# Kernel tuning notes

Measured on AMD Instinct MI355X. Metric: run time of the kernel, lower is better.

The kernel has to match this reference:

```python
import jax, jax.numpy as jnp
import numpy as np

SIMS = 16
AMP = 1.0  # cfg['attention_amplifier']


def setup_inputs() -> dict:
    key = jax.random.key(0)
    k1, k2, k3 = jax.random.split(key, 3)
    B, F = 32, 2048
    data = jax.random.normal(k1, (B * SIMS, F), dtype=jnp.float32)
    attention = jax.random.normal(k2, (B * SIMS, F), dtype=jnp.float32)
    W = jax.random.normal(k3, (SIMS, 2 * SIMS), dtype=jnp.float32) * (1.0 / np.sqrt(2 * SIMS))
    b = jnp.zeros((SIMS,), dtype=jnp.float32)
    return {"data": data, "attention": attention, "W": W, "b": b}


def reference(data, attention, W, b):
    s = SIMS
    B = data.shape[0] // s
    inputs = data.reshape(B, s, -1)            # [B, s, F]
    attn_in = attention.reshape(B, s, -1)      # [B, s, G]
    # bmm(inputs^T, attention) -> [B, F, G]
    a = jnp.einsum('bsf,bsg->bfg', inputs, attn_in)
    a = jax.nn.log_softmax(a, axis=1)          # log_softmax over F dim (dim=1)
    # bmm(a, attention^T) -> [B, F, s]
    a = jnp.einsum('bfg,bsg->bfs', a, attn_in)
    concat = jnp.concatenate([jnp.swapaxes(a, 1, 2), inputs], axis=1)  # [B, 2s, F]
    concat = jnp.swapaxes(concat, 1, 2).reshape(-1, 2 * s)             # [B*F, 2s]
    gate = jax.nn.sigmoid(concat @ W.T + b)    # [B*F, s]
    # output.t().contiguous().view(data.shape): [s, B*F] row-major -> [B*s, F]
    gate = gate.T.reshape(data.shape)
    return gate * data * AMP
```

## Files before the change

### kernel.cpp

```cpp
#include <hip/hip_runtime.h>
#include <math.h>

#define LOG2E 1.44269504088896340736f
#define LN2   0.69314718055994530942f

typedef _Float16 half8 __attribute__((ext_vector_type(8)));
typedef float f32x4v __attribute__((ext_vector_type(4)));

#define AROW 24

template <bool ATOMIC>
__global__ __launch_bounds__(256, 4) void kA(const float* __restrict__ data,
                                             const float* __restrict__ attn,
                                             float* __restrict__ Lout) {
    __shared__ _Float16 AhB[128 * AROW];
    __shared__ _Float16 AlB[128 * AROW];
    const int tid = threadIdx.x;
    const int b = blockIdx.z, fb = blockIdx.y, gb = blockIdx.x;
    const int wave = tid >> 6, lane = tid & 63;
    const int n = lane & 15, q = lane >> 4;
    const int s0 = (q & 1) * 8;

    const float* Tb = attn + (size_t)b * 16 * 2048;
    half8 B1[2], B2[2];
#pragma unroll
    for (int ct = 0; ct < 2; ++ct) {
        const int g = gb * 128 + wave * 32 + ct * 16 + n;
        half8 bh, bl;
#pragma unroll
        for (int j = 0; j < 8; ++j) {
            float x = Tb[(size_t)(s0 + j) * 2048 + g] * LOG2E;
            _Float16 h = (_Float16)x;
            _Float16 l = (_Float16)(x - (float)h);
            bh[j] = h;
            bl[j] = (q < 2) ? l : (_Float16)0.0f;
        }
        B1[ct] = bh;
        B2[ct] = bl;
    }

    f32x4v cs0 = {0.f, 0.f, 0.f, 0.f}, cs1 = {0.f, 0.f, 0.f, 0.f};

    const float* Ab = data + (size_t)b * 16 * 2048 + fb * 512;
    const int fst = tid & 127;
    const int sh  = (tid >> 7) * 8;
    const _Float16* aptr = ((q < 2) ? AhB : AlB) + n * AROW + s0;

    for (int chunk = 0; chunk < 4; ++chunk) {
        const float* Ac = Ab + chunk * 128;
        _Float16 hb[8], lb[8];
#pragma unroll
        for (int j = 0; j < 8; ++j) {
            float x = Ac[(size_t)(sh + j) * 2048 + fst];
            _Float16 h = (_Float16)x;
            hb[j] = h;
            lb[j] = (_Float16)(x - (float)h);
        }
        __syncthreads();
        half8 hv, lv;
#pragma unroll
        for (int j = 0; j < 8; ++j) { hv[j] = hb[j]; lv[j] = lb[j]; }
        *(half8*)(AhB + fst * AROW + sh) = hv;
        *(half8*)(AlB + fst * AROW + sh) = lv;
        __syncthreads();

#pragma unroll
        for (int rt = 0; rt < 8; ++rt) {
            half8 af = *(const half8*)(aptr + rt * 16 * AROW);
            f32x4v C = {0.f, 0.f, 0.f, 0.f};
            C = __builtin_amdgcn_mfma_f32_16x16x32_f16(af, B1[0], C, 0, 0, 0);
            C = __builtin_amdgcn_mfma_f32_16x16x32_f16(af, B2[0], C, 0, 0, 0);
            cs0[0] += __builtin_amdgcn_exp2f(C[0]);
            cs0[1] += __builtin_amdgcn_exp2f(C[1]);
            cs0[2] += __builtin_amdgcn_exp2f(C[2]);
            cs0[3] += __builtin_amdgcn_exp2f(C[3]);
            f32x4v D = {0.f, 0.f, 0.f, 0.f};
            D = __builtin_amdgcn_mfma_f32_16x16x32_f16(af, B1[1], D, 0, 0, 0);
            D = __builtin_amdgcn_mfma_f32_16x16x32_f16(af, B2[1], D, 0, 0, 0);
            cs1[0] += __builtin_amdgcn_exp2f(D[0]);
            cs1[1] += __builtin_amdgcn_exp2f(D[1]);
            cs1[2] += __builtin_amdgcn_exp2f(D[2]);
            cs1[3] += __builtin_amdgcn_exp2f(D[3]);
        }
    }

    float v0 = cs0[0] + cs0[1] + cs0[2] + cs0[3];
    float v1 = cs1[0] + cs1[1] + cs1[2] + cs1[3];
    v0 += __shfl_xor(v0, 16);
    v0 += __shfl_xor(v0, 32);
    v1 += __shfl_xor(v1, 16);
    v1 += __shfl_xor(v1, 32);
    if (q == 0) {
        const int g = gb * 128 + wave * 32 + n;
        if (ATOMIC) {
            atomicAdd(&Lout[(size_t)b * 2048 + g], v0);
            atomicAdd(&Lout[(size_t)b * 2048 + g + 16], v1);
        } else {
            Lout[((size_t)fb * 32 + b) * 2048 + g] = v0;
            Lout[((size_t)fb * 32 + b) * 2048 + g + 16] = v1;
        }
    }
}

#define TP 260
__global__ __launch_bounds__(256) void kTail(const float* __restrict__ attn,
                                             const float* __restrict__ Lpart, int nparts,
                                             float* __restrict__ Mpart,
                                             float* __restrict__ cpart) {
    __shared__ float Tsh[16 * TP];
    __shared__ float Lsh[256];
    __shared__ float red[16][17];
    const int tid = threadIdx.x;
    const int seg = blockIdx.x, b = blockIdx.y;
    const int g0 = seg * 256;

#pragma unroll
    for (int s = 0; s < 16; ++s)
        Tsh[s * TP + tid] = attn[(size_t)(b * 16 + s) * 2048 + g0 + tid];
    {
        float sum = 0.f;
        for (int p = 0; p < nparts; ++p)
            sum += Lpart[((size_t)p * 32 + b) * 2048 + g0 + tid];
        Lsh[tid] = LN2 * __builtin_amdgcn_logf(sum);
    }
    __syncthreads();

    {
        const int t = tid & 15, i = tid >> 4;
        float acc = 0.f;
#pragma unroll
        for (int k = 0; k < 4; ++k) {
            float4 l  = *(const float4*)(Lsh + i * 16 + k * 4);
            float4 tv = *(const float4*)(Tsh + t * TP + i * 16 + k * 4);
            acc += l.x * tv.x + l.y * tv.y + l.z * tv.z + l.w * tv.w;
        }
        red[t][i] = acc;
    }
    __syncthreads();
    if (tid < 16) {
        float s = 0.f;
#pragma unroll
        for (int k = 0; k < 16; ++k) s += red[tid][k];
        cpart[((size_t)seg * 32 + b) * 16 + tid] = s;
    }

    {
        const int s = tid >> 4, t = tid & 15;
        float a0 = 0.f, a1 = 0.f;
#pragma unroll 4
        for (int qk = 0; qk < 32; ++qk) {
            float4 x = *(const float4*)(Tsh + s * TP + qk * 8);
            float4 y = *(const float4*)(Tsh + t * TP + qk * 8);
            a0 += x.x * y.x + x.y * y.y + x.z * y.z + x.w * y.w;
            float4 x2 = *(const float4*)(Tsh + s * TP + qk * 8 + 4);
            float4 y2 = *(const float4*)(Tsh + t * TP + qk * 8 + 4);
            a1 += x2.x * y2.x + x2.y * y2.y + x2.z * y2.z + x2.w * y2.w;
        }
        Mpart[((size_t)seg * 32 + b) * 256 + tid] = a0 + a1;
    }
}

__global__ __launch_bounds__(256) void kC2(const float* __restrict__ data,
                                           const float* __restrict__ Mpart,
                                           const float* __restrict__ cpart,
                                           const float* __restrict__ W,
                                           const float* __restrict__ bias,
                                           float* __restrict__ out) {
    __shared__ float Msh[256];
    __shared__ float csh[16];
    __shared__ float Vsh[256];
    __shared__ float w0sh[16];
    const int tid = threadIdx.x;
    const int b = blockIdx.y;
    const int f = blockIdx.x * 256 + tid;

    {
        float m = 0.f;
#pragma unroll
        for (int p = 0; p < 8; ++p) m += Mpart[((size_t)p * 32 + b) * 256 + tid];
        Msh[tid] = m;
        if (tid < 16) {
            float c = 0.f;
#pragma unroll
            for (int p = 0; p < 8; ++p) c += cpart[((size_t)p * 32 + b) * 16 + tid];
            csh[tid] = c;
        }
    }
    __syncthreads();
    {
        const int s = tid >> 4, j = tid & 15;
        float acc = 0.f;
#pragma unroll
        for (int t = 0; t < 16; ++t) acc += Msh[s * 16 + t] * W[j * 32 + t];
        Vsh[s * 16 + j] = acc + W[j * 32 + 16 + s];
        if (s == 0) {
            float w0 = 0.f;
#pragma unroll
            for (int t = 0; t < 16; ++t) w0 += csh[t] * W[j * 32 + t];
            w0sh[j] = bias[j] - w0;
        }
    }
    __syncthreads();

    float As[16];
#pragma unroll
    for (int s = 0; s < 16; ++s)
        As[s] = data[(size_t)(b * 16 + s) * 2048 + f];
#pragma unroll
    for (int j = 0; j < 16; ++j) {
        float p = w0sh[j];
#pragma unroll
        for (int s = 0; s < 16; ++s) p += As[s] * Vsh[s * 16 + j];
        float e = __builtin_amdgcn_exp2f(-LOG2E * p);
        float gate = __builtin_amdgcn_rcpf(1.0f + e);
        size_t r = (size_t)(j * 32 + b) * 2048 + f;
        out[r] = gate * data[r];
    }
}

extern "C" void kernel_launch(void* const* d_in, const int* in_sizes, int n_in,
                              void* d_out, int out_size, void* d_ws, size_t ws_size,
                              hipStream_t stream) {
    const float* data = (const float*)d_in[0];
    const float* attn = (const float*)d_in[1];
    const float* W    = (const float*)d_in[2];
    const float* bias = (const float*)d_in[3];
    float* out = (float*)d_out;
    float* ws  = (float*)d_ws;

    const size_t LP = 4 * 32 * 2048;
    const size_t need_big = LP + 65536 + 4096;

    if (ws_size >= need_big * sizeof(float)) {
        float* Lpart = ws;
        float* Mpart = ws + LP;
        float* cpart = Mpart + 65536;
        kA<false><<<dim3(16, 4, 32), 256, 0, stream>>>(data, attn, Lpart);
        kTail<<<dim3(8, 32), 256, 0, stream>>>(attn, Lpart, 4, Mpart, cpart);
        kC2<<<dim3(8, 32), 256, 0, stream>>>(data, Mpart, cpart, W, bias, out);
    } else {
        float* Lsum  = ws;
        float* Mpart = ws + 65536;
        float* cpart = Mpart + 65536;
        hipMemsetAsync(Lsum, 0, 65536 * sizeof(float), stream);
        kA<true><<<dim3(16, 4, 32), 256, 0, stream>>>(data, attn, Lsum);
        kTail<<<dim3(8, 32), 256, 0, stream>>>(attn, Lsum, 1, Mpart, cpart);
        kC2<<<dim3(8, 32), 256, 0, stream>>>(data, Mpart, cpart, W, bias, out);
    }
}
```

Measured before the change: 94.99 us.

## Double-buffer LDS A tiles and widen kA to 256 columns per block

kA now covers 256 g-columns per block (4 column tiles per wave) instead of 128, which halves the grid and halves redundant loads and fp16 split conversion of the data tile. The shared A buffers become double-buffered so the next chunk's global load overlaps the MFMA and exp2 work on the current chunk, leaving one barrier per chunk. In exchange each thread holds more registers (B fragments, accumulators, prefetch), which may lower occupancy, and the smaller grid gives less parallelism.

After: 219.5 us. +131.0%, slower.

```diff
diff --git a/kernel.cpp b/kernel.cpp
--- a/kernel.cpp
+++ b/kernel.cpp
@@ -13,8 +13,8 @@
 __global__ __launch_bounds__(256, 4) void kA(const float* __restrict__ data,
                                              const float* __restrict__ attn,
                                              float* __restrict__ Lout) {
-    __shared__ _Float16 AhB[128 * AROW];
-    __shared__ _Float16 AlB[128 * AROW];
+    __shared__ _Float16 AhB[2][128 * AROW];
+    __shared__ _Float16 AlB[2][128 * AROW];
     const int tid = threadIdx.x;
     const int b = blockIdx.z, fb = blockIdx.y, gb = blockIdx.x;
     const int wave = tid >> 6, lane = tid & 63;
@@ -22,10 +22,10 @@
     const int s0 = (q & 1) * 8;
 
     const float* Tb = attn + (size_t)b * 16 * 2048;
-    half8 B1[2], B2[2];
-#pragma unroll
-    for (int ct = 0; ct < 2; ++ct) {
-        const int g = gb * 128 + wave * 32 + ct * 16 + n;
+    half8 B1[4], B2[4];
+#pragma unroll
+    for (int ct = 0; ct < 4; ++ct) {
+        const int g = gb * 256 + wave * 64 + ct * 16 + n;
         half8 bh, bl;
 #pragma unroll
         for (int j = 0; j < 8; ++j) {
@@ -39,65 +39,88 @@
         B2[ct] = bl;
     }
 
-    f32x4v cs0 = {0.f, 0.f, 0.f, 0.f}, cs1 = {0.f, 0.f, 0.f, 0.f};
+    f32x4v cs[4];
+#pragma unroll
+    for (int ct = 0; ct < 4; ++ct) cs[ct] = (f32x4v){0.f, 0.f, 0.f, 0.f};
 
     const float* Ab = data + (size_t)b * 16 * 2048 + fb * 512;
     const int fst = tid & 127;
     const int sh  = (tid >> 7) * 8;
-    const _Float16* aptr = ((q < 2) ? AhB : AlB) + n * AROW + s0;
-
-    for (int chunk = 0; chunk < 4; ++chunk) {
-        const float* Ac = Ab + chunk * 128;
-        _Float16 hb[8], lb[8];
+
+    const _Float16* ap0 = ((q < 2) ? &AhB[0][0] : &AlB[0][0]) + n * AROW + s0;
+    const _Float16* ap1 = ((q < 2) ? &AhB[1][0] : &AlB[1][0]) + n * AROW + s0;
+
+    {
+        const float* Ac = Ab;
+        half8 hv, lv;
 #pragma unroll
         for (int j = 0; j < 8; ++j) {
             float x = Ac[(size_t)(sh + j) * 2048 + fst];
             _Float16 h = (_Float16)x;
-            hb[j] = h;
-            lb[j] = (_Float16)(x - (float)h);
-        }
-        __syncthreads();
-        half8 hv, lv;
-#pragma unroll
-        for (int j = 0; j < 8; ++j) { hv[j] = hb[j]; lv[j] = lb[j]; }
-        *(half8*)(AhB + fst * AROW + sh) = hv;
-        *(half8*)(AlB + fst * AROW + sh) = lv;
-        __syncthreads();
-
+            hv[j] = h;
+            lv[j] = (_Float16)(x - (float)h);
+        }
+        *(half8*)(&AhB[0][fst * AROW + sh]) = hv;
+        *(half8*)(&AlB[0][fst * AROW + sh]) = lv;
+    }
+    __syncthreads();
+
+    for (int c = 0; c < 4; ++c) {
+        float xr[8];
+        if (c < 3) {
+            const float* Ac = Ab + (c + 1) * 128;
+#pragma unroll
+            for (int j = 0; j < 8; ++j)
+                xr[j] = Ac[(size_t)(sh + j) * 2048 + fst];
+        }
+
+        const _Float16* aptr = (c & 1) ? ap1 : ap0;
 #pragma unroll
         for (int rt = 0; rt < 8; ++rt) {
             half8 af = *(const half8*)(aptr + rt * 16 * AROW);
-            f32x4v C = {0.f, 0.f, 0.f, 0.f};
-            C = __builtin_amdgcn_mfma_f32_16x16x32_f16(af, B1[0], C, 0, 0, 0);
-            C = __builtin_amdgcn_mfma_f32_16x16x32_f16(af, B2[0], C, 0, 0, 0);
-            cs0[0] += __builtin_amdgcn_exp2f(C[0]);
-            cs0[1] += __builtin_amdgcn_exp2f(C[1]);
-            cs0[2] += __builtin_amdgcn_exp2f(C[2]);
-            cs0[3] += __builtin_amdgcn_exp2f(C[3]);
-            f32x4v D = {0.f, 0.f, 0.f, 0.f};
-            D = __builtin_amdgcn_mfma_f32_16x16x32_f16(af, B1[1], D, 0, 0, 0);
-            D = __builtin_amdgcn_mfma_f32_16x16x32_f16(af, B2[1], D, 0, 0, 0);
-            cs1[0] += __builtin_amdgcn_exp2f(D[0]);
-            cs1[1] += __builtin_amdgcn_exp2f(D[1]);
-            cs1[2] += __builtin_amdgcn_exp2f(D[2]);
-            cs1[3] += __builtin_amdgcn_exp2f(D[3]);
-        }
-    }
-
-    float v0 = cs0[0] + cs0[1] + cs0[2] + cs0[3];
-    float v1 = cs1[0] + cs1[1] + cs1[2] + cs1[3];
-    v0 += __shfl_xor(v0, 16);
-    v0 += __shfl_xor(v0, 32);
-    v1 += __shfl_xor(v1, 16);
-    v1 += __shfl_xor(v1, 32);
-    if (q == 0) {
-        const int g = gb * 128 + wave * 32 + n;
-        if (ATOMIC) {
-            atomicAdd(&Lout[(size_t)b * 2048 + g], v0);
-            atomicAdd(&Lout[(size_t)b * 2048 + g + 16], v1);
-        } else {
-            Lout[((size_t)fb * 32 + b) * 2048 + g] = v0;
-            Lout[((size_t)fb * 32 + b) * 2048 + g + 16] = v1;
+            f32x4v Cr[4];
+#pragma unroll
+            for (int ct = 0; ct < 4; ++ct) {
+                f32x4v t = {0.f, 0.f, 0.f, 0.f};
+                t = __builtin_amdgcn_mfma_f32_16x16x32_f16(af, B1[ct], t, 0, 0, 0);
+                t = __builtin_amdgcn_mfma_f32_16x16x32_f16(af, B2[ct], t, 0, 0, 0);
+                Cr[ct] = t;
+            }
+#pragma unroll
+            for (int ct = 0; ct < 4; ++ct) {
+                cs[ct][0] += __builtin_amdgcn_exp2f(Cr[ct][0]);
+                cs[ct][1] += __builtin_amdgcn_exp2f(Cr[ct][1]);
+                cs[ct][2] += __builtin_amdgcn_exp2f(Cr[ct][2]);
+                cs[ct][3] += __builtin_amdgcn_exp2f(Cr[ct][3]);
+            }
+        }
+
+        if (c < 3) {
+            half8 hv, lv;
+#pragma unroll
+            for (int j = 0; j < 8; ++j) {
+                _Float16 h = (_Float16)xr[j];
+                hv[j] = h;
+                lv[j] = (_Float16)(xr[j] - (float)h);
+            }
+            const int nb = (c + 1) & 1;
+            *(half8*)(&AhB[nb][fst * AROW + sh]) = hv;
+            *(half8*)(&AlB[nb][fst * AROW + sh]) = lv;
+        }
+        __syncthreads();
+    }
+
+#pragma unroll
+    for (int ct = 0; ct < 4; ++ct) {
+        float v = cs[ct][0] + cs[ct][1] + cs[ct][2] + cs[ct][3];
+        v += __shfl_xor(v, 16);
+        v += __shfl_xor(v, 32);
+        if (q == 0) {
+            const int g = gb * 256 + wave * 64 + ct * 16 + n;
+            if (ATOMIC)
+                atomicAdd(&Lout[(size_t)b * 2048 + g], v);
+            else
+                Lout[((size_t)fb * 32 + b) * 2048 + g] = v;
         }
     }
 }
@@ -235,7 +258,7 @@
         float* Lpart = ws;
         float* Mpart = ws + LP;
         float* cpart = Mpart + 65536;
-        kA<false><<<dim3(16, 4, 32), 256, 0, stream>>>(data, attn, Lpart);
+        kA<false><<<dim3(8, 4, 32), 256, 0, stream>>>(data, attn, Lpart);
         kTail<<<dim3(8, 32), 256, 0, stream>>>(attn, Lpart, 4, Mpart, cpart);
         kC2<<<dim3(8, 32), 256, 0, stream>>>(data, Mpart, cpart, W, bias, out);
     } else {
@@ -243,7 +266,7 @@
         float* Mpart = ws + 65536;
         float* cpart = Mpart + 65536;
         hipMemsetAsync(Lsum, 0, 65536 * sizeof(float), stream);
-        kA<true><<<dim3(16, 4, 32), 256, 0, stream>>>(data, attn, Lsum);
+        kA<true><<<dim3(8, 4, 32), 256, 0, stream>>>(data, attn, Lsum);
         kTail<<<dim3(8, 32), 256, 0, stream>>>(attn, Lsum, 1, Mpart, cpart);
         kC2<<<dim3(8, 32), 256, 0, stream>>>(data, Mpart, cpart, W, bias, out);
     }
```

## Swap operand residency in kA: keep data tile in registers, stage attention in LDS

Applied to the files above, without the earlier changes.

Restructures the log-sum-exp kernel so each wave holds its 64 rows of data (split into high and low fp16 parts) in registers, while a 256-column attention tile is staged once in LDS and streamed through. The grid changes from 16x4 to 8x8 tiles per batch, and the per-wave column sums are reduced through shared memory before one store per column. This removes the per-chunk data staging with its double barrier and spreads the exp work differently. In exchange it uses more LDS per block and produces eight partial buffers instead of four, so the tail kernel has more partials to reduce.

Measured after the change: 98.30 us. 1.03x slower.

```diff
diff --git a/kernel.cpp b/kernel.cpp
--- a/kernel.cpp
+++ b/kernel.cpp
@@ -7,98 +7,91 @@
 typedef _Float16 half8 __attribute__((ext_vector_type(8)));
 typedef float f32x4v __attribute__((ext_vector_type(4)));
 
-#define AROW 24
+#define TROW 24
 
 template <bool ATOMIC>
 __global__ __launch_bounds__(256, 4) void kA(const float* __restrict__ data,
                                              const float* __restrict__ attn,
                                              float* __restrict__ Lout) {
-    __shared__ _Float16 AhB[128 * AROW];
-    __shared__ _Float16 AlB[128 * AROW];
+    __shared__ _Float16 ThL[256 * TROW];
+    __shared__ _Float16 TlL[256 * TROW];
+    __shared__ _Float16 zeroH[8];
+    __shared__ float Lw[4][256];
     const int tid = threadIdx.x;
-    const int b = blockIdx.z, fb = blockIdx.y, gb = blockIdx.x;
+    const int b = blockIdx.z, fb = blockIdx.y, gs = blockIdx.x;
     const int wave = tid >> 6, lane = tid & 63;
     const int n = lane & 15, q = lane >> 4;
-    const int s0 = (q & 1) * 8;
-
-    const float* Tb = attn + (size_t)b * 16 * 2048;
-    half8 B1[2], B2[2];
-#pragma unroll
-    for (int ct = 0; ct < 2; ++ct) {
-        const int g = gb * 128 + wave * 32 + ct * 16 + n;
-        half8 bh, bl;
-#pragma unroll
-        for (int j = 0; j < 8; ++j) {
-            float x = Tb[(size_t)(s0 + j) * 2048 + g] * LOG2E;
-            _Float16 h = (_Float16)x;
-            _Float16 l = (_Float16)(x - (float)h);
-            bh[j] = h;
-            bl[j] = (q < 2) ? l : (_Float16)0.0f;
-        }
-        B1[ct] = bh;
-        B2[ct] = bl;
-    }
-
-    f32x4v cs0 = {0.f, 0.f, 0.f, 0.f}, cs1 = {0.f, 0.f, 0.f, 0.f};
-
-    const float* Ab = data + (size_t)b * 16 * 2048 + fb * 512;
-    const int fst = tid & 127;
-    const int sh  = (tid >> 7) * 8;
-    const _Float16* aptr = ((q < 2) ? AhB : AlB) + n * AROW + s0;
-
-    for (int chunk = 0; chunk < 4; ++chunk) {
-        const float* Ac = Ab + chunk * 128;
-        _Float16 hb[8], lb[8];
-#pragma unroll
-        for (int j = 0; j < 8; ++j) {
-            float x = Ac[(size_t)(sh + j) * 2048 + fst];
-            _Float16 h = (_Float16)x;
-            hb[j] = h;
-            lb[j] = (_Float16)(x - (float)h);
-        }
-        __syncthreads();
-        half8 hv, lv;
-#pragma unroll
-        for (int j = 0; j < 8; ++j) { hv[j] = hb[j]; lv[j] = lb[j]; }
-        *(half8*)(AhB + fst * AROW + sh) = hv;
-        *(half8*)(AlB + fst * AROW + sh) = lv;
-        __syncthreads();
-
-#pragma unroll
-        for (int rt = 0; rt < 8; ++rt) {
-            half8 af = *(const half8*)(aptr + rt * 16 * AROW);
+    const int g0 = gs * 256;
+
+    {
+        const float* Tb = attn + (size_t)b * 16 * 2048 + g0;
+        const int gl = tid >> 1;
+        const int sh = (tid & 1) * 8;
+#pragma unroll
+        for (int p = 0; p < 2; ++p) {
+            const int g = gl + p * 128;
+            half8 hv, lv;
+#pragma unroll
+            for (int j = 0; j < 8; ++j) {
+                float x = Tb[(size_t)(sh + j) * 2048 + g] * LOG2E;
+                _Float16 h = (_Float16)x;
+                hv[j] = h;
+                lv[j] = (_Float16)(x - (float)h);
+            }
+            *(half8*)(ThL + g * TROW + sh) = hv;
+            *(half8*)(TlL + g * TROW + sh) = lv;
+        }
+        if (tid < 8) zeroH[tid] = (_Float16)0.0f;
+    }
+
+    half8 A1[4];
+    {
+        const float* Ab = data + (size_t)b * 16 * 2048;
+        const int frow = fb * 256 + wave * 64;
+#pragma unroll
+        for (int r = 0; r < 4; ++r) {
+            half8 a;
+#pragma unroll
+            for (int j = 0; j < 8; ++j) {
+                const int s = (q & 1) * 8 + j;
+                float x = Ab[(size_t)s * 2048 + frow + r * 16 + n];
+                _Float16 h = (_Float16)x;
+                a[j] = (q < 2) ? h : (_Float16)(x - (float)h);
+            }
+            A1[r] = a;
+        }
+    }
+    __syncthreads();
+
+    const _Float16* b1base = ThL + (q & 1) * 8;
+    const _Float16* b2base = (q < 2) ? (TlL + q * 8) : zeroH;
+    const int b2stride = (q < 2) ? TROW : 0;
+
+    for (int gt = 0; gt < 16; ++gt) {
+        const int gp = gt * 16 + n;
+        half8 B1 = *(const half8*)(b1base + gp * TROW);
+        half8 B2 = *(const half8*)(b2base + gp * b2stride);
+        float sum = 0.f;
+#pragma unroll
+        for (int r = 0; r < 4; ++r) {
             f32x4v C = {0.f, 0.f, 0.f, 0.f};
-            C = __builtin_amdgcn_mfma_f32_16x16x32_f16(af, B1[0], C, 0, 0, 0);
-            C = __builtin_amdgcn_mfma_f32_16x16x32_f16(af, B2[0], C, 0, 0, 0);
-            cs0[0] += __builtin_amdgcn_exp2f(C[0]);
-            cs0[1] += __builtin_amdgcn_exp2f(C[1]);
-            cs0[2] += __builtin_amdgcn_exp2f(C[2]);
-            cs0[3] += __builtin_amdgcn_exp2f(C[3]);
-            f32x4v D = {0.f, 0.f, 0.f, 0.f};
-            D = __builtin_amdgcn_mfma_f32_16x16x32_f16(af, B1[1], D, 0, 0, 0);
-            D = __builtin_amdgcn_mfma_f32_16x16x32_f16(af, B2[1], D, 0, 0, 0);
-            cs1[0] += __builtin_amdgcn_exp2f(D[0]);
-            cs1[1] += __builtin_amdgcn_exp2f(D[1]);
-            cs1[2] += __builtin_amdgcn_exp2f(D[2]);
-            cs1[3] += __builtin_amdgcn_exp2f(D[3]);
-        }
-    }
-
-    float v0 = cs0[0] + cs0[1] + cs0[2] + cs0[3];
-    float v1 = cs1[0] + cs1[1] + cs1[2] + cs1[3];
-    v0 += __shfl_xor(v0, 16);
-    v0 += __shfl_xor(v0, 32);
-    v1 += __shfl_xor(v1, 16);
-    v1 += __shfl_xor(v1, 32);
-    if (q == 0) {
-        const int g = gb * 128 + wave * 32 + n;
-        if (ATOMIC) {
-            atomicAdd(&Lout[(size_t)b * 2048 + g], v0);
-            atomicAdd(&Lout[(size_t)b * 2048 + g + 16], v1);
-        } else {
-            Lout[((size_t)fb * 32 + b) * 2048 + g] = v0;
-            Lout[((size_t)fb * 32 + b) * 2048 + g + 16] = v1;
-        }
+            C = __builtin_amdgcn_mfma_f32_16x16x32_f16(A1[r], B1, C, 0, 0, 0);
+            C = __builtin_amdgcn_mfma_f32_16x16x32_f16(A1[r], B2, C, 0, 0, 0);
+            sum += __builtin_amdgcn_exp2f(C[0]) + __builtin_amdgcn_exp2f(C[1])
+                 + __builtin_amdgcn_exp2f(C[2]) + __builtin_amdgcn_exp2f(C[3]);
+        }
+        sum += __shfl_xor(sum, 16);
+        sum += __shfl_xor(sum, 32);
+        if (q == 0) Lw[wave][gp] = sum;
+    }
+    __syncthreads();
+
+    {
+        const float v = Lw[0][tid] + Lw[1][tid] + Lw[2][tid] + Lw[3][tid];
+        if (ATOMIC)
+            atomicAdd(&Lout[(size_t)b * 2048 + g0 + tid], v);
+        else
+            Lout[((size_t)fb * 32 + b) * 2048 + g0 + tid] = v;
     }
 }
 
@@ -228,22 +221,22 @@
     float* out = (float*)d_out;
     float* ws  = (float*)d_ws;
 
-    const size_t LP = 4 * 32 * 2048;
+    const size_t LP = 8 * 32 * 2048;
     const size_t need_big = LP + 65536 + 4096;
 
     if (ws_size >= need_big * sizeof(float)) {
         float* Lpart = ws;
         float* Mpart = ws + LP;
         float* cpart = Mpart + 65536;
-        kA<false><<<dim3(16, 4, 32), 256, 0, stream>>>(data, attn, Lpart);
-        kTail<<<dim3(8, 32), 256, 0, stream>>>(attn, Lpart, 4, Mpart, cpart);
+        kA<false><<<dim3(8, 8, 32), 256, 0, stream>>>(data, attn, Lpart);
+        kTail<<<dim3(8, 32), 256, 0, stream>>>(attn, Lpart, 8, Mpart, cpart);
         kC2<<<dim3(8, 32), 256, 0, stream>>>(data, Mpart, cpart, W, bias, out);
     } else {
         float* Lsum  = ws;
         float* Mpart = ws + 65536;
         float* cpart = Mpart + 65536;
         hipMemsetAsync(Lsum, 0, 65536 * sizeof(float), stream);
-        kA<true><<<dim3(16, 4, 32), 256, 0, stream>>>(data, attn, Lsum);
+        kA<true><<<dim3(8, 8, 32), 256, 0, stream>>>(data, attn, Lsum);
         kTail<<<dim3(8, 32), 256, 0, stream>>>(attn, Lsum, 1, Mpart, cpart);
         kC2<<<dim3(8, 32), 256, 0, stream>>>(data, Mpart, cpart, W, bias, out);
     }
```
